# Kernel optimization log

Measured on AMD Instinct MI355X. Metric: run time of the kernel, lower is better.

Reference implementation:

```python
import jax, jax.numpy as jnp
import numpy as np

S, B = 128, 1024          # num_segments, batch
DIM0, DIM1, DIM2 = 300, 74, 35
HID = 40                  # hidden_size -> reduced dims [40, 40, 35]
EMB = 256                 # embedded_dim (hard-coded in module)
M = 3                     # num_modality
TAU = 5.0                 # temperature
LSTM_IN = HID + HID + DIM2 + 2 * M  # 121


def setup_inputs() -> dict:
    key = jax.random.key(0)
    ks = jax.random.split(key, 16)
    rn = lambda k, shp, sc: jax.random.normal(k, shp, jnp.float32) * sc
    return {
        "x0": rn(ks[0], (S, B, DIM0), 1.0),
        "x1": rn(ks[1], (S, B, DIM1), 1.0),
        "x2": rn(ks[2], (S, B, DIM2), 1.0),
        "x_lens": jax.random.randint(ks[3], (B,), 1, S + 1),
        "gumbel_u": jax.random.uniform(ks[4], (S, M * B, 2), jnp.float32, 1e-6, 1.0 - 1e-6),
        # feature reduction (modality 2 is Identity since 35 == min(35, 40))
        "W0": rn(ks[5], (HID, DIM0), (1.0 / DIM0) ** 0.5),
        "b0": jnp.zeros((HID,), jnp.float32),
        "W1": rn(ks[6], (HID, DIM1), (1.0 / DIM1) ** 0.5),
        "b1": jnp.zeros((HID,), jnp.float32),
        # LSTMCell (PyTorch gate order i, f, g, o)
        "W_ih": rn(ks[7], (4 * EMB, LSTM_IN), (1.0 / LSTM_IN) ** 0.5),
        "W_hh": rn(ks[8], (4 * EMB, EMB), (1.0 / EMB) ** 0.5),
        "b_ih": jnp.zeros((4 * EMB,), jnp.float32),
        "b_hh": jnp.zeros((4 * EMB,), jnp.float32),
        # per-modality decision heads, stacked: [M, 2, EMB]
        "W_dec": rn(ks[9], (M, 2, EMB), (1.0 / EMB) ** 0.5),
        "b_dec": jnp.zeros((M, 2), jnp.float32),
    }


def reference(x0, x1, x2, x_lens, gumbel_u, W0, b0, W1, b1,
              W_ih, W_hh, b_ih, b_hh, W_dec, b_dec):
    del x_lens  # unused by the original forward
    # feature-dim reduction, then concat over modalities -> [S, B, 115]
    reduced = jnp.concatenate([x0 @ W0.T + b0, x1 @ W1.T + b1, x2], axis=-1)
    Bn = reduced.shape[1]
    h0 = jnp.zeros((Bn, EMB), reduced.dtype)
    c0 = jnp.zeros((Bn, EMB), reduced.dtype)
    p0 = jnp.zeros((Bn, 2 * M), reduced.dtype)  # prev-logits feedback, zeros at step 0

    def step(carry, inp):
        h, c, prev = carry
        r_i, u = inp                      # [B, 115], [M*B, 2]
        x = jnp.concatenate([r_i, prev], axis=-1)  # [B, 121]
        gates = x @ W_ih.T + b_ih + h @ W_hh.T + b_hh
        i_, f_, g_, o_ = jnp.split(gates, 4, axis=-1)
        c = jax.nn.sigmoid(f_) * c + jax.nn.sigmoid(i_) * jnp.tanh(g_)
        h = jax.nn.sigmoid(o_) * jnp.tanh(c)
        logits = jnp.einsum('bh,moh->mbo', h, W_dec) + b_dec[:, None, :]  # [M, B, 2]
        flat = logits.reshape(M * Bn, 2)  # == torch.cat(dim=0) of per-modality [B,2]
        g = -jnp.log(-jnp.log(u))         # Gumbel(0,1) noise
        y_soft = jax.nn.softmax((flat + g) / TAU, axis=-1)
        y_hard = jax.nn.one_hot(jnp.argmax(y_soft, axis=-1), 2, dtype=y_soft.dtype)
        y = y_soft + jax.lax.stop_gradient(y_hard - y_soft)  # straight-through hard
        decision = y[:, -1]               # [M*B]
        # logits.view(M,-1,2).permute(1,0,2).view(-1, 2M) -> [B, 2M]
        prev_next = logits.transpose(1, 0, 2).reshape(Bn, 2 * M)
        return (h, c, prev_next), (decision, logits)

    _, (dec, all_logits) = jax.lax.scan(step, (h0, c0, p0), (reduced, gumbel_u))
    decisions = dec.reshape(-1, M, Bn)    # [S, M, B]
    return decisions, all_logits          # [S, M, B], [S, M, B, 2]
```

## Files before the change

kernel.cpp:

```cpp
#include <hip/hip_runtime.h>
#include <math.h>

#define Sx 128
#define Bx 1024
#define D0x 300
#define D1x 74
#define D2x 35
#define HIDx 40
#define EMBx 256
#define Mx 3
#define KXx 115
#define KTOTx 371
#define KPADx 384
#define TAUx 5.0f

__global__ __launch_bounds__(256) void k_prep(
    const float* __restrict__ W0, const float* __restrict__ W1,
    const float* __restrict__ W_ih, const float* __restrict__ W_hh,
    const float* __restrict__ W_dec, const float* __restrict__ b_ih,
    const float* __restrict__ b_hh, const float* __restrict__ b_dec,
    float* __restrict__ Wt3, float* __restrict__ WTA, float* __restrict__ WTB,
    float* __restrict__ bias0, float* __restrict__ bias2) {
  int idx = blockIdx.x * 256 + threadIdx.x;
  if (idx < KPADx * 1024) {
    int k = idx >> 10, rem = idx & 1023;
    int dd = rem >> 2, q = rem & 3;
    int j = q * 256 + dd;
    float v = 0.f;
    if (k < KXx) {
      v = W_ih[j * 121 + k];
    } else if (k < KTOTx) {
      int kh = k - KXx;
      v = W_hh[j * 256 + kh];
#pragma unroll
      for (int p = 0; p < 6; ++p)
        v = fmaf(W_ih[j * 121 + 115 + p], W_dec[p * 256 + kh], v);
    }
    Wt3[idx] = v;
    return;
  }
  int r1 = idx - KPADx * 1024;
  if (r1 < 304 * 64) {
    int k = r1 >> 6, rem = r1 & 63;
    int txx = rem >> 2, q = rem & 3, c = q * 16 + txx;
    WTA[r1] = (c < 40 && k < 300) ? W0[c * 300 + k] : 0.f;
    return;
  }
  int r2 = r1 - 304 * 64;
  if (r2 < 76 * 64) {
    int k = r2 >> 6, rem = r2 & 63;
    int txx = rem >> 2, q = rem & 3, c = q * 16 + txx;
    WTB[r2] = (c < 40 && k < 74) ? W1[c * 74 + k] : 0.f;
    return;
  }
  int r3 = r2 - 76 * 64;
  if (r3 < 1024) {
    int j = r3;
    float b = b_ih[j] + b_hh[j];
    bias0[j] = b;
    float b2 = b;
#pragma unroll
    for (int p = 0; p < 6; ++p) b2 = fmaf(W_ih[j * 121 + 115 + p], b_dec[p], b2);
    bias2[j] = b2;
  }
}

__global__ __launch_bounds__(256) void k_copy_x2(const float* __restrict__ x2,
                                                 float* __restrict__ reduced) {
  int id = blockIdx.x * 256 + threadIdx.x;
  if (id >= Sx * Bx * D2x) return;
  int row = id / 35, jj = id - row * 35;
  reduced[(size_t)row * KXx + 80 + jj] = x2[id];
}

template <int MODE, int KB, int CSZ>
__device__ __forceinline__ void gemm_chunk(const float* __restrict__ Xa,
                                           const float* __restrict__ Xb,
                                           const float* __restrict__ WT,
                                           int r0, int d, int tid, int ty,
                                           float (&acc)[2][4], float (*xs)[196]) {
  constexpr int DCOLS = (MODE == 2) ? 256 : 16;
  constexpr int KD = (MODE == 0) ? 300 : ((MODE == 1) ? 74 : 0);
  constexpr int LDX = (MODE == 0) ? 300 : 74;
  for (int i = tid; i < 64 * CSZ; i += 512) {
    int r = i / CSZ, kk = i - r * CSZ, k = KB + kk;
    float v = 0.f;
    if constexpr (MODE == 2) {
      if (k < KXx) v = Xa[(size_t)(r0 + r) * KXx + k];
      else if (k < KTOTx) v = Xb[(size_t)(r0 + r) * EMBx + (k - KXx)];
    } else {
      if (k < KD) v = Xa[(size_t)(r0 + r) * LDX + k];
    }
    xs[r][kk] = v;
  }
  __syncthreads();
  const float* wp = WT + ((size_t)KB * DCOLS + d) * 4;
  for (int kk = 0; kk < CSZ; kk += 4) {
    float4 w0 = *(const float4*)(wp + (size_t)(kk + 0) * DCOLS * 4);
    float4 w1 = *(const float4*)(wp + (size_t)(kk + 1) * DCOLS * 4);
    float4 w2 = *(const float4*)(wp + (size_t)(kk + 2) * DCOLS * 4);
    float4 w3 = *(const float4*)(wp + (size_t)(kk + 3) * DCOLS * 4);
#pragma unroll
    for (int rr = 0; rr < 2; ++rr) {
      float4 xv = *(const float4*)(&xs[ty * 2 + rr][kk]);
      acc[rr][0] = fmaf(xv.x, w0.x, acc[rr][0]);
      acc[rr][1] = fmaf(xv.x, w0.y, acc[rr][1]);
      acc[rr][2] = fmaf(xv.x, w0.z, acc[rr][2]);
      acc[rr][3] = fmaf(xv.x, w0.w, acc[rr][3]);
      acc[rr][0] = fmaf(xv.y, w1.x, acc[rr][0]);
      acc[rr][1] = fmaf(xv.y, w1.y, acc[rr][1]);
      acc[rr][2] = fmaf(xv.y, w1.z, acc[rr][2]);
      acc[rr][3] = fmaf(xv.y, w1.w, acc[rr][3]);
      acc[rr][0] = fmaf(xv.z, w2.x, acc[rr][0]);
      acc[rr][1] = fmaf(xv.z, w2.y, acc[rr][1]);
      acc[rr][2] = fmaf(xv.z, w2.z, acc[rr][2]);
      acc[rr][3] = fmaf(xv.z, w2.w, acc[rr][3]);
      acc[rr][0] = fmaf(xv.w, w3.x, acc[rr][0]);
      acc[rr][1] = fmaf(xv.w, w3.y, acc[rr][1]);
      acc[rr][2] = fmaf(xv.w, w3.z, acc[rr][2]);
      acc[rr][3] = fmaf(xv.w, w3.w, acc[rr][3]);
    }
  }
}

template <int MODE>
__global__ __launch_bounds__(512) void k_gemm(const float* __restrict__ Xa,
                                              const float* __restrict__ Xb,
                                              const float* __restrict__ WT,
                                              const float* __restrict__ bias,
                                              float* __restrict__ outp,
                                              float* __restrict__ cbuf) {
  __shared__ __align__(16) float xs[64][196];
  constexpr int CS0 = (MODE == 1) ? 76 : 192;
  constexpr int CS1 = (MODE == 0) ? 112 : ((MODE == 1) ? 0 : 180);

  int bid = blockIdx.x;
  int r0, d0;
  if constexpr (MODE == 2) { r0 = (bid >> 4) * 64; d0 = (bid & 15) * 16; }
  else { r0 = bid * 64; d0 = 0; }
  int tid = threadIdx.x;
  int tx = tid & 15, ty = tid >> 4;
  int d = d0 + tx;
  float acc[2][4] = {{0.f, 0.f, 0.f, 0.f}, {0.f, 0.f, 0.f, 0.f}};

  gemm_chunk<MODE, 0, CS0>(Xa, Xb, WT, r0, d, tid, ty, acc, xs);
  if constexpr (CS1 > 0) {
    __syncthreads();
    gemm_chunk<MODE, CS0, CS1>(Xa, Xb, WT, r0, d, tid, ty, acc, xs);
  }

  if constexpr (MODE == 2) {
#pragma unroll
    for (int rr = 0; rr < 2; ++rr) {
      int row = r0 + ty * 2 + rr;
      float iv = acc[rr][0] + bias[d];
      float fv = acc[rr][1] + bias[256 + d];
      float gv = acc[rr][2] + bias[512 + d];
      float ov = acc[rr][3] + bias[768 + d];
      float si = 1.f / (1.f + expf(-iv));
      float sf = 1.f / (1.f + expf(-fv));
      float so = 1.f / (1.f + expf(-ov));
      float tg = tanhf(gv);
      size_t ci = (size_t)row * EMBx + d;
      float cn = __fadd_rn(__fmul_rn(sf, cbuf[ci]), __fmul_rn(si, tg));
      cbuf[ci] = cn;
      outp[ci] = __fmul_rn(so, tanhf(cn));
    }
  } else {
    constexpr int OFF = (MODE == 0) ? 0 : 40;
#pragma unroll
    for (int rr = 0; rr < 2; ++rr) {
      int row = r0 + ty * 2 + rr;
#pragma unroll
      for (int q = 0; q < 4; ++q) {
        int c = q * 16 + tx;
        if (c < 40) outp[(size_t)row * KXx + OFF + c] = acc[rr][q] + bias[c];
      }
    }
  }
}

__global__ __launch_bounds__(256) void k_out(const float* __restrict__ hbase,
                                             const float* __restrict__ W_dec,
                                             const float* __restrict__ b_dec,
                                             const float* __restrict__ gu,
                                             float* __restrict__ outp,
                                             int s_start, int nrows) {
  int lane = threadIdx.x & 63;
  int row = blockIdx.x * 4 + (threadIdx.x >> 6);
  if (row >= nrows) return;
  int s = s_start + (row >> 10), b = row & 1023;
  const float* h = hbase + (size_t)row * EMBx;
  float4 hv = *(const float4*)(h + lane * 4);
  float a[6];
#pragma unroll
  for (int p = 0; p < 6; ++p) {
    float4 wv = *(const float4*)(W_dec + p * EMBx + lane * 4);
    a[p] = hv.x * wv.x + hv.y * wv.y + hv.z * wv.z + hv.w * wv.w;
  }
#pragma unroll
  for (int p = 0; p < 6; ++p) {
#pragma unroll
    for (int off = 32; off > 0; off >>= 1) a[p] += __shfl_xor(a[p], off, 64);
  }
  if (lane < 6) {
    int m = lane >> 1, o = lane & 1;
    outp[(size_t)Sx * Mx * Bx + (((size_t)(s * Mx + m) * Bx + b) << 1) + o] =
        a[lane] + b_dec[lane];
  }
  if (lane < 3) {
    int m = lane;
    float l0 = a[2 * m] + b_dec[2 * m];
    float l1 = a[2 * m + 1] + b_dec[2 * m + 1];
    const float* up = gu + (((size_t)s * 3072 + m * 1024 + b) << 1);
    float g0 = -logf(-logf(up[0]));
    float g1 = -logf(-logf(up[1]));
    float v0 = (l0 + g0) / TAUx;
    float v1 = (l1 + g1) / TAUx;
    outp[(size_t)s * Mx * Bx + m * Bx + b] = (v1 > v0) ? 1.0f : 0.0f;
  }
}

extern "C" void kernel_launch(void* const* d_in, const int* in_sizes, int n_in,
                              void* d_out, int out_size, void* d_ws, size_t ws_size,
                              hipStream_t stream) {
  const float* x0 = (const float*)d_in[0];
  const float* x1 = (const float*)d_in[1];
  const float* x2 = (const float*)d_in[2];
  const float* gu = (const float*)d_in[4];
  const float* W0 = (const float*)d_in[5];
  const float* b0 = (const float*)d_in[6];
  const float* W1 = (const float*)d_in[7];
  const float* b1 = (const float*)d_in[8];
  const float* W_ih = (const float*)d_in[9];
  const float* W_hh = (const float*)d_in[10];
  const float* b_ih = (const float*)d_in[11];
  const float* b_hh = (const float*)d_in[12];
  const float* W_dec = (const float*)d_in[13];
  const float* b_dec = (const float*)d_in[14];
  float* outp = (float*)d_out;

  float* ws = (float*)d_ws;
  float* Wt3 = ws;
  float* WTA = Wt3 + 393216;
  float* WTB = WTA + 19456;
  float* bias0 = WTB + 4864;
  float* bias2 = bias0 + 1024;
  float* cbuf = bias2 + 1024;
  float* reduced = cbuf + 262144;
  float* hall = reduced + (size_t)15073280;

  size_t base_f = 393216 + 19456 + 4864 + 1024 + 1024 + 262144 + (size_t)15073280;
  size_t need_full = (base_f + (size_t)129 * 262144) * 4;
  bool full = ws_size >= need_full;

  hipMemsetAsync(cbuf, 0, 262144 * 4, stream);
  hipMemsetAsync(hall, 0, 262144 * 4, stream);

  k_prep<<<1635, 256, 0, stream>>>(W0, W1, W_ih, W_hh, W_dec, b_ih, b_hh, b_dec,
                                   Wt3, WTA, WTB, bias0, bias2);
  k_gemm<0><<<2048, 512, 0, stream>>>(x0, nullptr, WTA, b0, reduced, nullptr);
  k_gemm<1><<<2048, 512, 0, stream>>>(x1, nullptr, WTB, b1, reduced, nullptr);
  k_copy_x2<<<(Sx * Bx * D2x + 255) / 256, 256, 0, stream>>>(x2, reduced);

  for (int t = 0; t < Sx; ++t) {
    const float* hin;
    float* hout;
    if (full) {
      hin = hall + (size_t)t * 262144;
      hout = hall + (size_t)(t + 1) * 262144;
    } else {
      hin = hall + (size_t)(t & 1) * 262144;
      hout = hall + (size_t)((t + 1) & 1) * 262144;
    }
    k_gemm<2><<<256, 512, 0, stream>>>(reduced + (size_t)t * Bx * KXx, hin, Wt3,
                                       (t == 0) ? bias0 : bias2, hout, cbuf);
    if (!full) {
      k_out<<<256, 256, 0, stream>>>(hout, W_dec, b_dec, gu, outp, t, Bx);
    }
  }
  if (full) {
    k_out<<<(Sx * Bx) / 4, 256, 0, stream>>>(hall + 262144, W_dec, b_dec, gu,
                                             outp, 0, Sx * Bx);
  }
}
```

Measured before the change: 7.271 ms.

## Fuse LSTM timesteps into one persistent kernel with per-group grid barriers

Replaces the 128 per-step GEMM launches plus the output kernel with a single persistent kernel. Each block keeps its weight slice in shared memory and its cell state in registers, double-buffers the input staging, and synchronizes the 16 blocks that share a batch group through an atomic counter barrier. The decision-head logits and Gumbel decisions are computed inside the same step. The input-reduction GEMMs now stage weights in LDS and fold the x2 copy into the mode-1 kernel. The cost is a spin barrier that relies on all 256 blocks being co-resident, so the kernel can deadlock if occupancy is insufficient.

```diff
diff --git a/kernel.cpp b/kernel.cpp
--- a/kernel.cpp
+++ b/kernel.cpp
@@ -3,16 +3,13 @@
 
 #define Sx 128
 #define Bx 1024
-#define D0x 300
-#define D1x 74
-#define D2x 35
-#define HIDx 40
 #define EMBx 256
 #define Mx 3
 #define KXx 115
 #define KTOTx 371
-#define KPADx 384
+#define RSTR 120
 #define TAUx 5.0f
+#define DEC_SZ (Sx * Mx * Bx)
 
 __global__ __launch_bounds__(256) void k_prep(
     const float* __restrict__ W0, const float* __restrict__ W1,
@@ -22,7 +19,7 @@
     float* __restrict__ Wt3, float* __restrict__ WTA, float* __restrict__ WTB,
     float* __restrict__ bias0, float* __restrict__ bias2) {
   int idx = blockIdx.x * 256 + threadIdx.x;
-  if (idx < KPADx * 1024) {
+  if (idx < 384 * 1024) {
     int k = idx >> 10, rem = idx & 1023;
     int dd = rem >> 2, q = rem & 3;
     int j = q * 256 + dd;
@@ -39,7 +36,7 @@
     Wt3[idx] = v;
     return;
   }
-  int r1 = idx - KPADx * 1024;
+  int r1 = idx - 384 * 1024;
   if (r1 < 304 * 64) {
     int k = r1 >> 6, rem = r1 & 63;
     int txx = rem >> 2, q = rem & 3, c = q * 16 + txx;
@@ -65,44 +62,38 @@
   }
 }
 
-__global__ __launch_bounds__(256) void k_copy_x2(const float* __restrict__ x2,
-                                                 float* __restrict__ reduced) {
-  int id = blockIdx.x * 256 + threadIdx.x;
-  if (id >= Sx * Bx * D2x) return;
-  int row = id / 35, jj = id - row * 35;
-  reduced[(size_t)row * KXx + 80 + jj] = x2[id];
-}
-
-template <int MODE, int KB, int CSZ>
-__device__ __forceinline__ void gemm_chunk(const float* __restrict__ Xa,
-                                           const float* __restrict__ Xb,
-                                           const float* __restrict__ WT,
-                                           int r0, int d, int tid, int ty,
-                                           float (&acc)[2][4], float (*xs)[196]) {
-  constexpr int DCOLS = (MODE == 2) ? 256 : 16;
-  constexpr int KD = (MODE == 0) ? 300 : ((MODE == 1) ? 74 : 0);
-  constexpr int LDX = (MODE == 0) ? 300 : 74;
-  for (int i = tid; i < 64 * CSZ; i += 512) {
-    int r = i / CSZ, kk = i - r * CSZ, k = KB + kk;
-    float v = 0.f;
-    if constexpr (MODE == 2) {
-      if (k < KXx) v = Xa[(size_t)(r0 + r) * KXx + k];
-      else if (k < KTOTx) v = Xb[(size_t)(r0 + r) * EMBx + (k - KXx)];
-    } else {
-      if (k < KD) v = Xa[(size_t)(r0 + r) * LDX + k];
-    }
-    xs[r][kk] = v;
-  }
+template <int MODE>
+__global__ __launch_bounds__(512) void k_in(const float* __restrict__ X,
+                                            const float* __restrict__ x2,
+                                            const float* __restrict__ WT,
+                                            const float* __restrict__ bias,
+                                            float* __restrict__ red) {
+  constexpr int KD = (MODE == 0) ? 300 : 74;
+  constexpr int KP = (MODE == 0) ? 304 : 76;
+  constexpr int OFF = (MODE == 0) ? 0 : 40;
+  __shared__ __align__(16) float xs[64][KP];
+  __shared__ __align__(16) float wl[KP * 64];
+
+  int r0 = blockIdx.x * 64;
+  int tid = threadIdx.x, tx = tid & 15, ty = tid >> 4;
+
+  for (int i = tid; i < 64 * KP; i += 512) {
+    int r = i / KP, k = i - r * KP;
+    xs[r][k] = (k < KD) ? X[(size_t)(r0 + r) * KD + k] : 0.f;
+  }
+  for (int i = tid; i < KP * 64; i += 512) wl[i] = WT[i];
   __syncthreads();
-  const float* wp = WT + ((size_t)KB * DCOLS + d) * 4;
-  for (int kk = 0; kk < CSZ; kk += 4) {
-    float4 w0 = *(const float4*)(wp + (size_t)(kk + 0) * DCOLS * 4);
-    float4 w1 = *(const float4*)(wp + (size_t)(kk + 1) * DCOLS * 4);
-    float4 w2 = *(const float4*)(wp + (size_t)(kk + 2) * DCOLS * 4);
-    float4 w3 = *(const float4*)(wp + (size_t)(kk + 3) * DCOLS * 4);
+
+  float acc[2][4] = {{0.f, 0.f, 0.f, 0.f}, {0.f, 0.f, 0.f, 0.f}};
+#pragma unroll 4
+  for (int kk = 0; kk < KP; kk += 4) {
+    float4 w0 = *(const float4*)&wl[(kk + 0) * 64 + tx * 4];
+    float4 w1 = *(const float4*)&wl[(kk + 1) * 64 + tx * 4];
+    float4 w2 = *(const float4*)&wl[(kk + 2) * 64 + tx * 4];
+    float4 w3 = *(const float4*)&wl[(kk + 3) * 64 + tx * 4];
 #pragma unroll
     for (int rr = 0; rr < 2; ++rr) {
-      float4 xv = *(const float4*)(&xs[ty * 2 + rr][kk]);
+      float4 xv = *(const float4*)&xs[ty * 2 + rr][kk];
       acc[rr][0] = fmaf(xv.x, w0.x, acc[rr][0]);
       acc[rr][1] = fmaf(xv.x, w0.y, acc[rr][1]);
       acc[rr][2] = fmaf(xv.x, w0.z, acc[rr][2]);
@@ -121,103 +112,186 @@
       acc[rr][3] = fmaf(xv.w, w3.w, acc[rr][3]);
     }
   }
-}
-
-template <int MODE>
-__global__ __launch_bounds__(512) void k_gemm(const float* __restrict__ Xa,
-                                              const float* __restrict__ Xb,
-                                              const float* __restrict__ WT,
-                                              const float* __restrict__ bias,
-                                              float* __restrict__ outp,
-                                              float* __restrict__ cbuf) {
-  __shared__ __align__(16) float xs[64][196];
-  constexpr int CS0 = (MODE == 1) ? 76 : 192;
-  constexpr int CS1 = (MODE == 0) ? 112 : ((MODE == 1) ? 0 : 180);
-
-  int bid = blockIdx.x;
-  int r0, d0;
-  if constexpr (MODE == 2) { r0 = (bid >> 4) * 64; d0 = (bid & 15) * 16; }
-  else { r0 = bid * 64; d0 = 0; }
-  int tid = threadIdx.x;
-  int tx = tid & 15, ty = tid >> 4;
+#pragma unroll
+  for (int rr = 0; rr < 2; ++rr) {
+    int row = r0 + ty * 2 + rr;
+#pragma unroll
+    for (int q = 0; q < 4; ++q) {
+      int c = q * 16 + tx;
+      if (c < 40) red[(size_t)row * RSTR + OFF + c] = acc[rr][q] + bias[c];
+    }
+  }
+  if constexpr (MODE == 1) {
+    for (int i = tid; i < 64 * 40; i += 512) {
+      int r = i / 40, c = i - r * 40;
+      red[(size_t)(r0 + r) * RSTR + 80 + c] =
+          (c < 35) ? x2[(size_t)(r0 + r) * 35 + c] : 0.f;
+    }
+  }
+}
+
+__device__ __forceinline__ void stage(float (*dst)[96], const float* __restrict__ redt,
+                                      const float* __restrict__ hprev, int kbase,
+                                      int r0, int tid) {
+  for (int i = tid; i < 64 * 96; i += 512) {
+    int r = i / 96, kk = i - r * 96, k = kbase + kk;
+    float v = 0.f;
+    if (k < KXx)
+      v = redt[(size_t)(r0 + r) * RSTR + k];
+    else if (k < KTOTx && hprev)
+      v = hprev[(size_t)(r0 + r) * EMBx + (k - KXx)];
+    dst[r][kk] = v;
+  }
+}
+
+template <int NQ>
+__device__ __forceinline__ void compute(float (&acc)[2][4], const float (*xb)[96],
+                                        const float* __restrict__ wl, int kbase,
+                                        int tx, int ty) {
+#pragma unroll 8
+  for (int kk = 0; kk < NQ; ++kk) {
+    int k = kbase + kk * 4;
+    float4 w0 = *(const float4*)&wl[(k + 0) * 64 + tx * 4];
+    float4 w1 = *(const float4*)&wl[(k + 1) * 64 + tx * 4];
+    float4 w2 = *(const float4*)&wl[(k + 2) * 64 + tx * 4];
+    float4 w3 = *(const float4*)&wl[(k + 3) * 64 + tx * 4];
+#pragma unroll
+    for (int rr = 0; rr < 2; ++rr) {
+      float4 xv = *(const float4*)&xb[ty * 2 + rr][kk * 4];
+      acc[rr][0] = fmaf(xv.x, w0.x, acc[rr][0]);
+      acc[rr][1] = fmaf(xv.x, w0.y, acc[rr][1]);
+      acc[rr][2] = fmaf(xv.x, w0.z, acc[rr][2]);
+      acc[rr][3] = fmaf(xv.x, w0.w, acc[rr][3]);
+      acc[rr][0] = fmaf(xv.y, w1.x, acc[rr][0]);
+      acc[rr][1] = fmaf(xv.y, w1.y, acc[rr][1]);
+      acc[rr][2] = fmaf(xv.y, w1.z, acc[rr][2]);
+      acc[rr][3] = fmaf(xv.y, w1.w, acc[rr][3]);
+      acc[rr][0] = fmaf(xv.z, w2.x, acc[rr][0]);
+      acc[rr][1] = fmaf(xv.z, w2.y, acc[rr][1]);
+      acc[rr][2] = fmaf(xv.z, w2.z, acc[rr][2]);
+      acc[rr][3] = fmaf(xv.z, w2.w, acc[rr][3]);
+      acc[rr][0] = fmaf(xv.w, w3.x, acc[rr][0]);
+      acc[rr][1] = fmaf(xv.w, w3.y, acc[rr][1]);
+      acc[rr][2] = fmaf(xv.w, w3.z, acc[rr][2]);
+      acc[rr][3] = fmaf(xv.w, w3.w, acc[rr][3]);
+    }
+  }
+}
+
+__global__ __launch_bounds__(512, 2) void k_lstm(
+    const float* __restrict__ red, const float* __restrict__ Wt3,
+    const float* __restrict__ bias0, const float* __restrict__ bias2,
+    const float* __restrict__ W_dec, const float* __restrict__ b_dec,
+    const float* __restrict__ gu, float* __restrict__ hbuf,
+    int* __restrict__ bar, float* __restrict__ outp) {
+  __shared__ __align__(16) float wl[372 * 64];
+  __shared__ __align__(16) float xl[2][64][96];
+
+  int b = blockIdx.x;
+  int g = b >> 4, ct = b & 15;
+  int r0 = g * 64, d0 = ct * 16;
+  int tid = threadIdx.x, tx = tid & 15, ty = tid >> 4;
   int d = d0 + tx;
-  float acc[2][4] = {{0.f, 0.f, 0.f, 0.f}, {0.f, 0.f, 0.f, 0.f}};
-
-  gemm_chunk<MODE, 0, CS0>(Xa, Xb, WT, r0, d, tid, ty, acc, xs);
-  if constexpr (CS1 > 0) {
-    __syncthreads();
-    gemm_chunk<MODE, CS0, CS1>(Xa, Xb, WT, r0, d, tid, ty, acc, xs);
-  }
-
-  if constexpr (MODE == 2) {
+
+  for (int i = tid; i < 372 * 64; i += 512) {
+    int k = i >> 6, j = i & 63;
+    wl[i] = Wt3[(size_t)k * 1024 + d0 * 4 + j];
+  }
+  float b0r[4], b2r[4];
+#pragma unroll
+  for (int q = 0; q < 4; ++q) {
+    b0r[q] = bias0[q * 256 + d];
+    b2r[q] = bias2[q * 256 + d];
+  }
+  float creg[2] = {0.f, 0.f};
+
+  const float* hprev = hbuf;
+  float* hcur = hbuf + 262144;
+
+  stage(xl[0], red, nullptr, 0, r0, tid);
+  __syncthreads();
+
+  for (int t = 0; t < Sx; ++t) {
+    const float* redt = red + (size_t)t * Bx * RSTR;
+    float acc[2][4] = {{0.f, 0.f, 0.f, 0.f}, {0.f, 0.f, 0.f, 0.f}};
+
+    stage(xl[1], redt, hprev, 96, r0, tid);
+    compute<24>(acc, xl[0], wl, 0, tx, ty);
+    __syncthreads();
+    stage(xl[0], redt, hprev, 192, r0, tid);
+    compute<24>(acc, xl[1], wl, 96, tx, ty);
+    __syncthreads();
+    stage(xl[1], redt, hprev, 288, r0, tid);
+    compute<24>(acc, xl[0], wl, 192, tx, ty);
+    __syncthreads();
+    if (t < Sx - 1)
+      stage(xl[0], red + (size_t)(t + 1) * Bx * RSTR, nullptr, 0, r0, tid);
+    compute<21>(acc, xl[1], wl, 288, tx, ty);
+
 #pragma unroll
     for (int rr = 0; rr < 2; ++rr) {
       int row = r0 + ty * 2 + rr;
-      float iv = acc[rr][0] + bias[d];
-      float fv = acc[rr][1] + bias[256 + d];
-      float gv = acc[rr][2] + bias[512 + d];
-      float ov = acc[rr][3] + bias[768 + d];
+      float iv = acc[rr][0] + ((t == 0) ? b0r[0] : b2r[0]);
+      float fv = acc[rr][1] + ((t == 0) ? b0r[1] : b2r[1]);
+      float gv = acc[rr][2] + ((t == 0) ? b0r[2] : b2r[2]);
+      float ov = acc[rr][3] + ((t == 0) ? b0r[3] : b2r[3]);
       float si = 1.f / (1.f + expf(-iv));
       float sf = 1.f / (1.f + expf(-fv));
       float so = 1.f / (1.f + expf(-ov));
       float tg = tanhf(gv);
-      size_t ci = (size_t)row * EMBx + d;
-      float cn = __fadd_rn(__fmul_rn(sf, cbuf[ci]), __fmul_rn(si, tg));
-      cbuf[ci] = cn;
-      outp[ci] = __fmul_rn(so, tanhf(cn));
-    }
-  } else {
-    constexpr int OFF = (MODE == 0) ? 0 : 40;
-#pragma unroll
-    for (int rr = 0; rr < 2; ++rr) {
-      int row = r0 + ty * 2 + rr;
-#pragma unroll
-      for (int q = 0; q < 4; ++q) {
-        int c = q * 16 + tx;
-        if (c < 40) outp[(size_t)row * KXx + OFF + c] = acc[rr][q] + bias[c];
+      float cn = __fadd_rn(__fmul_rn(sf, creg[rr]), __fmul_rn(si, tg));
+      creg[rr] = cn;
+      hcur[(size_t)row * EMBx + d] = __fmul_rn(so, tanhf(cn));
+    }
+
+    __threadfence();
+    __syncthreads();
+    if (tid == 0) {
+      atomicAdd(bar + g, 1);
+      while (__hip_atomic_load(bar + g, __ATOMIC_ACQUIRE,
+                               __HIP_MEMORY_SCOPE_AGENT) < 16 * (t + 1))
+        __builtin_amdgcn_s_sleep(2);
+    }
+    __syncthreads();
+    __threadfence();
+
+    {
+      int grp = tid >> 4, lane = tid & 15;
+      if (grp < 24) {
+        int r = grp / 6, p = grp - r * 6;
+        int row = r0 + ct * 4 + r;
+        const float* hr = hcur + (size_t)row * EMBx + lane * 16;
+        const float* wd = W_dec + p * EMBx + lane * 16;
+        float s = 0.f;
+#pragma unroll
+        for (int jj = 0; jj < 4; ++jj) {
+          float4 hv = *(const float4*)(hr + jj * 4);
+          float4 wv = *(const float4*)(wd + jj * 4);
+          s += hv.x * wv.x + hv.y * wv.y + hv.z * wv.z + hv.w * wv.w;
+        }
+        s += __shfl_xor(s, 1);
+        s += __shfl_xor(s, 2);
+        s += __shfl_xor(s, 4);
+        s += __shfl_xor(s, 8);
+        float logit = s + b_dec[p];
+        int m = p >> 1, o = p & 1;
+        if (lane == 0)
+          outp[DEC_SZ + (((size_t)(t * Mx + m) * Bx + row) << 1) + o] = logit;
+        float other = __shfl_xor(logit, 16);
+        if (lane == 0 && o == 0) {
+          const float* up = gu + (((size_t)t * 3072 + m * 1024 + row) << 1);
+          float g0 = -logf(-logf(up[0]));
+          float g1 = -logf(-logf(up[1]));
+          float v0 = (logit + g0) / TAUx;
+          float v1 = (other + g1) / TAUx;
+          outp[(size_t)t * 3072 + m * 1024 + row] = (v1 > v0) ? 1.0f : 0.0f;
+        }
       }
     }
-  }
-}
-
-__global__ __launch_bounds__(256) void k_out(const float* __restrict__ hbase,
-                                             const float* __restrict__ W_dec,
-                                             const float* __restrict__ b_dec,
-                                             const float* __restrict__ gu,
-                                             float* __restrict__ outp,
-                                             int s_start, int nrows) {
-  int lane = threadIdx.x & 63;
-  int row = blockIdx.x * 4 + (threadIdx.x >> 6);
-  if (row >= nrows) return;
-  int s = s_start + (row >> 10), b = row & 1023;
-  const float* h = hbase + (size_t)row * EMBx;
-  float4 hv = *(const float4*)(h + lane * 4);
-  float a[6];
-#pragma unroll
-  for (int p = 0; p < 6; ++p) {
-    float4 wv = *(const float4*)(W_dec + p * EMBx + lane * 4);
-    a[p] = hv.x * wv.x + hv.y * wv.y + hv.z * wv.z + hv.w * wv.w;
-  }
-#pragma unroll
-  for (int p = 0; p < 6; ++p) {
-#pragma unroll
-    for (int off = 32; off > 0; off >>= 1) a[p] += __shfl_xor(a[p], off, 64);
-  }
-  if (lane < 6) {
-    int m = lane >> 1, o = lane & 1;
-    outp[(size_t)Sx * Mx * Bx + (((size_t)(s * Mx + m) * Bx + b) << 1) + o] =
-        a[lane] + b_dec[lane];
-  }
-  if (lane < 3) {
-    int m = lane;
-    float l0 = a[2 * m] + b_dec[2 * m];
-    float l1 = a[2 * m + 1] + b_dec[2 * m + 1];
-    const float* up = gu + (((size_t)s * 3072 + m * 1024 + b) << 1);
-    float g0 = -logf(-logf(up[0]));
-    float g1 = -logf(-logf(up[1]));
-    float v0 = (l0 + g0) / TAUx;
-    float v1 = (l1 + g1) / TAUx;
-    outp[(size_t)s * Mx * Bx + m * Bx + b] = (v1 > v0) ? 1.0f : 0.0f;
+
+    float* tmp = (float*)hprev;
+    hprev = hcur;
+    hcur = (t & 1) ? hbuf + 262144 : hbuf;
   }
 }
 
@@ -246,41 +320,17 @@
   float* WTB = WTA + 19456;
   float* bias0 = WTB + 4864;
   float* bias2 = bias0 + 1024;
-  float* cbuf = bias2 + 1024;
-  float* reduced = cbuf + 262144;
-  float* hall = reduced + (size_t)15073280;
-
-  size_t base_f = 393216 + 19456 + 4864 + 1024 + 1024 + 262144 + (size_t)15073280;
-  size_t need_full = (base_f + (size_t)129 * 262144) * 4;
-  bool full = ws_size >= need_full;
-
-  hipMemsetAsync(cbuf, 0, 262144 * 4, stream);
-  hipMemsetAsync(hall, 0, 262144 * 4, stream);
+  int* bar = (int*)(bias2 + 1024);
+  float* hbuf = bias2 + 1024 + 64;
+  float* reduced = hbuf + 524288;
+
+  hipMemsetAsync(bar, 0, 64 * sizeof(int), stream);
+  hipMemsetAsync(hbuf, 0, 262144 * sizeof(float), stream);
 
   k_prep<<<1635, 256, 0, stream>>>(W0, W1, W_ih, W_hh, W_dec, b_ih, b_hh, b_dec,
                                    Wt3, WTA, WTB, bias0, bias2);
-  k_gemm<0><<<2048, 512, 0, stream>>>(x0, nullptr, WTA, b0, reduced, nullptr);
-  k_gemm<1><<<2048, 512, 0, stream>>>(x1, nullptr, WTB, b1, reduced, nullptr);
-  k_copy_x2<<<(Sx * Bx * D2x + 255) / 256, 256, 0, stream>>>(x2, reduced);
-
-  for (int t = 0; t < Sx; ++t) {
-    const float* hin;
-    float* hout;
-    if (full) {
-      hin = hall + (size_t)t * 262144;
-      hout = hall + (size_t)(t + 1) * 262144;
-    } else {
-      hin = hall + (size_t)(t & 1) * 262144;
-      hout = hall + (size_t)((t + 1) & 1) * 262144;
-    }
-    k_gemm<2><<<256, 512, 0, stream>>>(reduced + (size_t)t * Bx * KXx, hin, Wt3,
-                                       (t == 0) ? bias0 : bias2, hout, cbuf);
-    if (!full) {
-      k_out<<<256, 256, 0, stream>>>(hout, W_dec, b_dec, gu, outp, t, Bx);
-    }
-  }
-  if (full) {
-    k_out<<<(Sx * Bx) / 4, 256, 0, stream>>>(hall + 262144, W_dec, b_dec, gu,
-                                             outp, 0, Sx * Bx);
-  }
-}
+  k_in<0><<<2048, 512, 0, stream>>>(x0, nullptr, WTA, b0, reduced);
+  k_in<1><<<2048, 512, 0, stream>>>(x1, x2, WTB, b1, reduced);
+  k_lstm<<<256, 512, 0, stream>>>(reduced, Wt3, bias0, bias2, W_dec, b_dec, gu,
+                                  hbuf, bar, outp);
+}
```

Result: slower. 15.96 ms (+119.5%).
